# Optimization experiments

Hardware: AMD Instinct MI355X
Metric: run time of the kernel (lower is better)

The kernel has to match this reference:

```python
import jax, jax.numpy as jnp
import numpy as np

B, T, D_MODEL = 4, 2048, 2048
H, KV, HD = 16, 8, 128  # num_heads, num_kv_heads, head_dim
EPS = 1e-6


def _rope_tables(T, hd, base=10000.0):
    inv_freq = 1.0 / (base ** (np.arange(0, hd, 2, dtype=np.float32) / hd))  # [hd/2]
    ang = np.arange(T, dtype=np.float32)[:, None] * inv_freq[None, :]        # [T, hd/2]
    cos = np.repeat(np.cos(ang), 2, axis=-1)                                 # [T, hd]
    sin = np.repeat(np.sin(ang), 2, axis=-1)
    return jnp.asarray(cos), jnp.asarray(sin)


def setup_inputs() -> dict:
    key = jax.random.key(0)
    ks = jax.random.split(key, 6)
    w_std = 0.02
    x = jax.random.normal(ks[0], (B, T, D_MODEL), dtype=jnp.float32)
    Wq = jax.random.normal(ks[1], (D_MODEL, H * HD), dtype=jnp.float32) * w_std
    Wk = jax.random.normal(ks[2], (D_MODEL, KV * HD), dtype=jnp.float32) * w_std
    Wv = jax.random.normal(ks[3], (D_MODEL, KV * HD), dtype=jnp.float32) * w_std
    Wo = jax.random.normal(ks[4], (H * HD, D_MODEL), dtype=jnp.float32) * w_std
    cos, sin = _rope_tables(T, HD)
    q_gamma = jnp.ones((HD,), dtype=jnp.float32)
    k_gamma = jnp.ones((HD,), dtype=jnp.float32)
    return {"x": x, "cos": cos, "sin": sin, "Wq": Wq, "Wk": Wk, "Wv": Wv,
            "Wo": Wo, "q_gamma": q_gamma, "k_gamma": k_gamma}


def _rmsnorm(h, gamma):
    # flax nn.RMSNorm over last axis, learnable scale
    var = jnp.mean(h * h, axis=-1, keepdims=True)
    return h * jax.lax.rsqrt(var + EPS) * gamma


def _rope(h, cos, sin):
    # h: [B, T, heads, HD]; interleaved rotation
    h_rot = jnp.stack([-h[..., 1::2], h[..., 0::2]], axis=-1)
    h_rot = h_rot.reshape(h.shape)
    return h * cos[None, :, None, :] + h_rot * sin[None, :, None, :]


def reference(x, cos, sin, Wq, Wk, Wv, Wo, q_gamma, k_gamma):
    Bx, Tx, _ = x.shape
    G = H // KV  # query groups per kv head
    q = (x @ Wq).reshape(Bx, Tx, H, HD)
    k = (x @ Wk).reshape(Bx, Tx, KV, HD)
    v = (x @ Wv).reshape(Bx, Tx, KV, HD)
    q = _rope(_rmsnorm(q, q_gamma), cos, sin)
    k = _rope(_rmsnorm(k, k_gamma), cos, sin)
    scale = 1.0 / jnp.sqrt(jnp.asarray(HD, dtype=x.dtype))
    qg = q.reshape(Bx, Tx, KV, G, HD)
    # scores: [B, KV, G, Tq, Tk]
    scores = jnp.einsum('btkgd,bskd->bkgts', qg, k) * scale
    p = jax.nn.softmax(scores, axis=-1)
    o = jnp.einsum('bkgts,bskd->btkgd', p, v).reshape(Bx, Tx, H * HD)
    return o @ Wo
```

## Files before the change

### kernel.cpp

```cpp
#include <hip/hip_runtime.h>


typedef unsigned short u16;
typedef unsigned int u32;
typedef __attribute__((ext_vector_type(8))) short bf16x8;
typedef __attribute__((ext_vector_type(4))) float f32x4;

__device__ __forceinline__ float bf2f(u16 v) {
    union { u32 u; float f; } x; x.u = ((u32)v) << 16; return x.f;
}
__device__ __forceinline__ u16 f2bf(float f) {
    union { float f; u32 u; } x; x.f = f;
    u32 u = x.u;
    return (u16)((u + 0x7FFFu + ((u >> 16) & 1u)) >> 16);
}
__device__ __forceinline__ u32 packtrunc(float a, float b) {
    union { float f; u32 u; } x, y; x.f = a; y.f = b;
    return (x.u >> 16) | (y.u & 0xffff0000u);
}
__device__ __forceinline__ f32x4 mfma_bf16(bf16x8 a, bf16x8 b, f32x4 c) {
    return __builtin_amdgcn_mfma_f32_16x16x32_bf16(a, b, c, 0, 0, 0);
}
__device__ __forceinline__ void gl_lds16(const u16* g, u16* l) {
    __builtin_amdgcn_global_load_lds((const __attribute__((address_space(1))) void*)g,
                                     (__attribute__((address_space(3))) void*)l, 16, 0, 0);
}

__global__ __launch_bounds__(256)
void transpose_f2b(const float* __restrict__ in, u16* __restrict__ out, int R, int C) {
    __shared__ float tile[32][33];
    const int tx = threadIdx.x & 31, ty = threadIdx.x >> 5;
    const long c0 = (long)blockIdx.x * 32, r0 = (long)blockIdx.y * 32;
#pragma unroll
    for (int i = 0; i < 4; i++)
        tile[ty + i * 8][tx] = in[(r0 + ty + i * 8) * C + c0 + tx];
    __syncthreads();
#pragma unroll
    for (int i = 0; i < 4; i++)
        out[(c0 + ty + i * 8) * R + r0 + tx] = f2bf(tile[tx][ty + i * 8]);
}

__global__ __launch_bounds__(256)
void cast_f2b(const float* __restrict__ in, u16* __restrict__ out) {
    const long i = ((long)blockIdx.x * 256 + threadIdx.x) * 8;
    float4 a = *(const float4*)(in + i);
    float4 b = *(const float4*)(in + i + 4);
    bf16x8 v;
    v[0] = (short)f2bf(a.x); v[1] = (short)f2bf(a.y);
    v[2] = (short)f2bf(a.z); v[3] = (short)f2bf(a.w);
    v[4] = (short)f2bf(b.x); v[5] = (short)f2bf(b.y);
    v[6] = (short)f2bf(b.z); v[7] = (short)f2bf(b.w);
    *(bf16x8*)(out + i) = v;
}

__global__ __launch_bounds__(256)
void transpose_v(const u16* __restrict__ qkv, u16* __restrict__ Vt) {
    __shared__ u16 tile[32][33];
    const int tx = threadIdx.x & 31, ty = threadIdx.x >> 5;
    const int d0 = blockIdx.x * 32;
    const int tok0 = blockIdx.y * 32;
#pragma unroll
    for (int i = 0; i < 4; i++)
        tile[ty + i * 8][tx] = qkv[(long)(tok0 + ty + i * 8) * 4096 + 3072 + d0 + tx];
    __syncthreads();
    const int b = tok0 >> 11;
    const long orow = (long)b * 1024 + d0;
    const int t0 = tok0 & 2047;
#pragma unroll
    for (int i = 0; i < 4; i++)
        Vt[(orow + ty + i * 8) * 2048 + t0 + tx] = tile[tx][ty + i * 8];
}

template <bool F32OUT>
__global__ __launch_bounds__(256)
void gemm_bt_bf16(const u16* __restrict__ A, const u16* __restrict__ Bt,
                  void* __restrict__ Cp, int M, int N, int K) {
    __shared__ __align__(16) u16 As[128 * 32];
    __shared__ __align__(16) u16 Bs[128 * 32];
    const int tid = threadIdx.x, wid = tid >> 6, lane = tid & 63;
    const int q4 = lane >> 4, n16 = lane & 15;
    const int wr = (wid >> 1) * 64, wc = (wid & 1) * 64;
    const long rowT = (long)blockIdx.y * 128, colT = (long)blockIdx.x * 128;

    const int srow = wid * 32 + (lane >> 2);
    const int scol = (lane & 3) * 8;
    const u16* Ag0 = A + (rowT + srow) * K + scol;
    const u16* Ag1 = Ag0 + (long)16 * K;
    const u16* Bg0 = Bt + (colT + srow) * K + scol;
    const u16* Bg1 = Bg0 + (long)16 * K;
    u16* la0 = As + wid * 1024 + lane * 8;
    u16* la1 = la0 + 512;
    u16* lb0 = Bs + wid * 1024 + lane * 8;
    u16* lb1 = lb0 + 512;

    f32x4 acc[4][4];
#pragma unroll
    for (int i = 0; i < 4; i++)
#pragma unroll
        for (int j = 0; j < 4; j++) acc[i][j] = (f32x4){0.f, 0.f, 0.f, 0.f};

    for (int k0 = 0; k0 < K; k0 += 32) {
        gl_lds16(Ag0 + k0, la0);
        gl_lds16(Ag1 + k0, la1);
        gl_lds16(Bg0 + k0, lb0);
        gl_lds16(Bg1 + k0, lb1);
        __syncthreads();
        bf16x8 af[4], bfr[4];
#pragma unroll
        for (int mb = 0; mb < 4; mb++) af[mb]  = *(const bf16x8*)&As[(wr + mb * 16 + n16) * 32 + q4 * 8];
#pragma unroll
        for (int nb = 0; nb < 4; nb++) bfr[nb] = *(const bf16x8*)&Bs[(wc + nb * 16 + n16) * 32 + q4 * 8];
#pragma unroll
        for (int mb = 0; mb < 4; mb++)
#pragma unroll
            for (int nb = 0; nb < 4; nb++)
                acc[mb][nb] = mfma_bf16(af[mb], bfr[nb], acc[mb][nb]);
        __syncthreads();
    }

#pragma unroll
    for (int mb = 0; mb < 4; mb++)
#pragma unroll
        for (int nb = 0; nb < 4; nb++)
#pragma unroll
            for (int r = 0; r < 4; r++) {
                long row = rowT + wr + mb * 16 + q4 * 4 + r;
                long col = colT + wc + nb * 16 + n16;
                if (F32OUT) ((float*)Cp)[row * N + col] = acc[mb][nb][r];
                else        ((u16*)Cp)[row * N + col]   = f2bf(acc[mb][nb][r]);
            }
}

__global__ __launch_bounds__(256)
void rmsnorm_rope(u16* __restrict__ qkv, const float* __restrict__ cosT,
                  const float* __restrict__ sinT, const float* __restrict__ qg,
                  const float* __restrict__ kg) {
    const int w = blockIdx.x * 4 + (threadIdx.x >> 6);
    const int lane = threadIdx.x & 63;
    const int token = w / 24;
    const int hv = w - token * 24;
    const long base = (long)token * 4096 + (hv < 16 ? hv * 128 : 2048 + (hv - 16) * 128);
    const float* g = (hv < 16) ? qg : kg;
    const int t = token & 2047;

    u32 pair = *(const u32*)(qkv + base + 2 * lane);
    float a0 = bf2f((u16)(pair & 0xffffu));
    float a1 = bf2f((u16)(pair >> 16));
    float ss = a0 * a0 + a1 * a1;
#pragma unroll
    for (int off = 32; off > 0; off >>= 1) ss += __shfl_xor(ss, off);
    float rs = rsqrtf(ss * (1.0f / 128.0f) + 1e-6f);
    float h0 = a0 * rs * g[2 * lane];
    float h1 = a1 * rs * g[2 * lane + 1];
    float2 cp = *(const float2*)(cosT + (long)t * 128 + 2 * lane);
    float2 sp = *(const float2*)(sinT + (long)t * 128 + 2 * lane);
    float o0 = h0 * cp.x - h1 * sp.x;
    float o1 = h1 * cp.y + h0 * sp.y;
    if (hv < 16) {
        const float QS = 0.08838834764831845f * 1.4426950408889634f;
        o0 *= QS; o1 *= QS;
    }
    *(u32*)(qkv + base + 2 * lane) = ((u32)f2bf(o0)) | (((u32)f2bf(o1)) << 16);
}

__global__ __launch_bounds__(256)
void flash_attn(const u16* __restrict__ qkv, const u16* __restrict__ Vt,
                u16* __restrict__ attn) {
    __shared__ __align__(16) u16 Ks[2][64 * 128];
    __shared__ __align__(16) u16 Vs[2][128 * 64];
    const int tid = threadIdx.x, wid = tid >> 6, lane = tid & 63;
    const int q4 = lane >> 4, n16 = lane & 15;
    const int b = blockIdx.y >> 4, h = blockIdx.y & 15;
    const int kvh = h >> 1;
    const long rowbase = (long)b * 2048;
    const long qbase = rowbase + (long)blockIdx.x * 128 + wid * 32;

    const u16* Kbase = qkv + rowbase * 4096 + 2048 + kvh * 128;
    const u16* Vbase = Vt + ((long)(b * 8 + kvh) * 128) * 2048;

    const int krow_off = lane >> 4;
    const int kslot = lane & 15;
    int ktr[4], kgc[4];
#pragma unroll
    for (int i = 0; i < 4; i++) {
        int rho = wid * 16 + i * 4 + krow_off;
        ktr[i] = (rho & 32) | ((rho & 12) << 1) | ((rho & 16) >> 2) | (rho & 3);
        kgc[i] = kslot ^ (rho & 7);
    }
    const int vrow_off = lane >> 3;
    const int vslot = lane & 7;
    const int vg = vslot ^ vrow_off;

    auto stage = [&](int buf, int kt) {
#pragma unroll
        for (int i = 0; i < 4; i++)
            gl_lds16(Kbase + (long)(kt + ktr[i]) * 4096 + kgc[i] * 8,
                     &Ks[buf][(wid * 16 + i * 4) * 128 + lane * 8]);
#pragma unroll
        for (int i = 0; i < 4; i++) {
            int d = wid * 32 + i * 8 + vrow_off;
            gl_lds16(Vbase + (long)d * 2048 + kt + vg * 8,
                     &Vs[buf][(wid * 32 + i * 8) * 64 + lane * 8]);
        }
    };

    bf16x8 qf[2][4];
#pragma unroll
    for (int qb = 0; qb < 2; qb++) {
        const u16* p = qkv + (qbase + qb * 16 + n16) * 4096 + h * 128;
#pragma unroll
        for (int c = 0; c < 4; c++) qf[qb][c] = *(const bf16x8*)(p + c * 32 + q4 * 8);
    }

    f32x4 o[2][8];
#pragma unroll
    for (int i = 0; i < 2; i++)
#pragma unroll
        for (int j = 0; j < 8; j++) o[i][j] = (f32x4){0.f, 0.f, 0.f, 0.f};
    float l_i[2] = {0.f, 0.f};
    const float SHIFT = 18.0f;

    const int swz = n16 & 7;

    stage(0, 0);
    asm volatile("s_waitcnt vmcnt(0)" ::: "memory");
    __builtin_amdgcn_s_barrier();

    int cur = 0;
    for (int kt = 0; kt < 2048; kt += 64) {
        if (kt + 64 < 2048) stage(cur ^ 1, kt + 64);

        const u16* KsC = Ks[cur];
        const u16* VsC = Vs[cur];

        f32x4 s[2][4];
#pragma unroll
        for (int qb = 0; qb < 2; qb++)
#pragma unroll
            for (int kb = 0; kb < 4; kb++) s[qb][kb] = (f32x4){0.f, 0.f, 0.f, 0.f};
#pragma unroll
        for (int c = 0; c < 4; c++) {
            bf16x8 kf[4];
#pragma unroll
            for (int kb = 0; kb < 4; kb++) {
                int slot = (c * 4 + q4) ^ swz;
                kf[kb] = *(const bf16x8*)&KsC[(kb * 16 + n16) * 128 + slot * 8];
            }
            __builtin_amdgcn_s_setprio(1);
#pragma unroll
            for (int qb = 0; qb < 2; qb++)
#pragma unroll
                for (int kb = 0; kb < 4; kb++)
                    s[qb][kb] = mfma_bf16(kf[kb], qf[qb][c], s[qb][kb]);
            __builtin_amdgcn_s_setprio(0);
        }

        u32 pw[2][8];
#pragma unroll
        for (int qb = 0; qb < 2; qb++) {
            float sum = 0.f;
#pragma unroll
            for (int kb = 0; kb < 4; kb++) {
                float p0 = exp2f(s[qb][kb][0] - SHIFT);
                float p1 = exp2f(s[qb][kb][1] - SHIFT);
                float p2 = exp2f(s[qb][kb][2] - SHIFT);
                float p3 = exp2f(s[qb][kb][3] - SHIFT);
                sum += (p0 + p1) + (p2 + p3);
                pw[qb][kb * 2]     = packtrunc(p0, p1);
                pw[qb][kb * 2 + 1] = packtrunc(p2, p3);
            }
            l_i[qb] += sum;
        }

#pragma unroll
        for (int kc = 0; kc < 2; kc++) {
            bf16x8 vf[8];
#pragma unroll
            for (int nbh = 0; nbh < 8; nbh++) {
                int slot = (kc * 4 + q4) ^ swz;
                vf[nbh] = *(const bf16x8*)&VsC[(nbh * 16 + n16) * 64 + slot * 8];
            }
            __builtin_amdgcn_s_setprio(1);
#pragma unroll
            for (int qb = 0; qb < 2; qb++) {
                union { u32 w[4]; bf16x8 v; } pu;
                pu.w[0] = pw[qb][kc * 4];
                pu.w[1] = pw[qb][kc * 4 + 1];
                pu.w[2] = pw[qb][kc * 4 + 2];
                pu.w[3] = pw[qb][kc * 4 + 3];
#pragma unroll
                for (int nbh = 0; nbh < 8; nbh++)
                    o[qb][nbh] = mfma_bf16(pu.v, vf[nbh], o[qb][nbh]);
            }
            __builtin_amdgcn_s_setprio(0);
        }

        asm volatile("s_waitcnt vmcnt(0)" ::: "memory");
        __builtin_amdgcn_s_barrier();
        cur ^= 1;
    }

#pragma unroll
    for (int qb = 0; qb < 2; qb++) {
        l_i[qb] += __shfl_xor(l_i[qb], 16);
        l_i[qb] += __shfl_xor(l_i[qb], 32);
    }

#pragma unroll
    for (int qb = 0; qb < 2; qb++) {
        float linv = 1.0f / l_i[qb];
        float l4[4];
#pragma unroll
        for (int r = 0; r < 4; r++)
            l4[r] = __shfl(linv, (lane & 48) | (q4 * 4 + r));
#pragma unroll
        for (int r = 0; r < 4; r++) {
            u16* op = attn + (qbase + qb * 16 + q4 * 4 + r) * 2048 + h * 128 + n16;
#pragma unroll
            for (int nbh = 0; nbh < 8; nbh++)
                op[nbh * 16] = f2bf(o[qb][nbh][r] * l4[r]);
        }
    }
}

extern "C" void kernel_launch(void* const* d_in, const int* in_sizes, int n_in,
                              void* d_out, int out_size, void* d_ws, size_t ws_size,
                              hipStream_t stream) {
    const float* x    = (const float*)d_in[0];
    const float* cosT = (const float*)d_in[1];
    const float* sinT = (const float*)d_in[2];
    const float* Wq   = (const float*)d_in[3];
    const float* Wk   = (const float*)d_in[4];
    const float* Wv   = (const float*)d_in[5];
    const float* Wo   = (const float*)d_in[6];
    const float* qg   = (const float*)d_in[7];
    const float* kg   = (const float*)d_in[8];
    float* out = (float*)d_out;

    char* ws = (char*)d_ws;
    u16* Bt_qkv = (u16*)(ws);
    u16* Vt     = (u16*)(ws);
    u16* Bt_o   = (u16*)(ws + 16777216);
    u16* xb     = (u16*)(ws + 25165824);
    u16* attn   = (u16*)(ws + 25165824);
    u16* qkv    = (u16*)(ws + 58720256);

    transpose_f2b<<<dim3(64, 64), 256, 0, stream>>>(Wq, Bt_qkv, 2048, 2048);
    transpose_f2b<<<dim3(32, 64), 256, 0, stream>>>(Wk, Bt_qkv + (size_t)2048 * 2048, 2048, 1024);
    transpose_f2b<<<dim3(32, 64), 256, 0, stream>>>(Wv, Bt_qkv + (size_t)3072 * 2048, 2048, 1024);
    transpose_f2b<<<dim3(64, 64), 256, 0, stream>>>(Wo, Bt_o, 2048, 2048);
    cast_f2b<<<dim3(8192), 256, 0, stream>>>(x, xb);

    gemm_bt_bf16<false><<<dim3(32, 64), 256, 0, stream>>>(xb, Bt_qkv, qkv, 8192, 4096, 2048);

    transpose_v<<<dim3(32, 256), 256, 0, stream>>>(qkv, Vt);
    rmsnorm_rope<<<dim3(49152), 256, 0, stream>>>(qkv, cosT, sinT, qg, kg);

    flash_attn<<<dim3(16, 64), 256, 0, stream>>>(qkv, Vt, attn);

    gemm_bt_bf16<true><<<dim3(16, 64), 256, 0, stream>>>(attn, Bt_o, out, 8192, 2048, 2048);
}
```

Measured before the change: 644.0 us.

## Replace 128x128 GEMM with double-buffered swizzled 256x256 tile GEMM

Result: faster. 574.6 us (-10.8%).

```diff
diff --git a/kernel.cpp b/kernel.cpp
--- a/kernel.cpp
+++ b/kernel.cpp
@@ -72,54 +72,83 @@
 }
 
 template <bool F32OUT>
-__global__ __launch_bounds__(256)
-void gemm_bt_bf16(const u16* __restrict__ A, const u16* __restrict__ Bt,
-                  void* __restrict__ Cp, int M, int N, int K) {
-    __shared__ __align__(16) u16 As[128 * 32];
-    __shared__ __align__(16) u16 Bs[128 * 32];
+__global__ __launch_bounds__(512, 2)
+void gemm_bt_256(const u16* __restrict__ A, const u16* __restrict__ Bt,
+                 void* __restrict__ Cp, int M, int N, int K) {
+    __shared__ __align__(16) u16 As[2][256 * 64];
+    __shared__ __align__(16) u16 Bs[2][256 * 64];
     const int tid = threadIdx.x, wid = tid >> 6, lane = tid & 63;
     const int q4 = lane >> 4, n16 = lane & 15;
-    const int wr = (wid >> 1) * 64, wc = (wid & 1) * 64;
-    const long rowT = (long)blockIdx.y * 128, colT = (long)blockIdx.x * 128;
-
-    const int srow = wid * 32 + (lane >> 2);
-    const int scol = (lane & 3) * 8;
-    const u16* Ag0 = A + (rowT + srow) * K + scol;
-    const u16* Ag1 = Ag0 + (long)16 * K;
-    const u16* Bg0 = Bt + (colT + srow) * K + scol;
-    const u16* Bg1 = Bg0 + (long)16 * K;
-    u16* la0 = As + wid * 1024 + lane * 8;
-    u16* la1 = la0 + 512;
-    u16* lb0 = Bs + wid * 1024 + lane * 8;
-    u16* lb1 = lb0 + 512;
-
-    f32x4 acc[4][4];
-#pragma unroll
-    for (int i = 0; i < 4; i++)
+    const int wr = (wid >> 2) * 128;
+    const int wc = (wid & 3) * 64;
+
+    const int nbx = N >> 8;
+    const int nwg = nbx * (M >> 8);
+    int id = (int)blockIdx.x;
+    id = (id & 7) * (nwg >> 3) + (id >> 3);
+    const long rowT = (long)(id / nbx) * 256;
+    const long colT = (long)(id % nbx) * 256;
+
+    const int srow = tid >> 3;
+    const int gchunk = (tid & 7) ^ (srow & 7);
+    const u16* Ag[4]; const u16* Bg[4];
+#pragma unroll
+    for (int i = 0; i < 4; i++) {
+        Ag[i] = A  + (rowT + i * 64 + srow) * K + gchunk * 8;
+        Bg[i] = Bt + (colT + i * 64 + srow) * K + gchunk * 8;
+    }
+    const int ldst = wid * 512 + lane * 8;
+
+    auto stage = [&](int buf, int kt) {
+#pragma unroll
+        for (int i = 0; i < 4; i++)
+            gl_lds16(Ag[i] + kt, &As[buf][i * 4096 + ldst]);
+#pragma unroll
+        for (int i = 0; i < 4; i++)
+            gl_lds16(Bg[i] + kt, &Bs[buf][i * 4096 + ldst]);
+    };
+
+    f32x4 acc[8][4];
+#pragma unroll
+    for (int i = 0; i < 8; i++)
 #pragma unroll
         for (int j = 0; j < 4; j++) acc[i][j] = (f32x4){0.f, 0.f, 0.f, 0.f};
 
-    for (int k0 = 0; k0 < K; k0 += 32) {
-        gl_lds16(Ag0 + k0, la0);
-        gl_lds16(Ag1 + k0, la1);
-        gl_lds16(Bg0 + k0, lb0);
-        gl_lds16(Bg1 + k0, lb1);
-        __syncthreads();
-        bf16x8 af[4], bfr[4];
-#pragma unroll
-        for (int mb = 0; mb < 4; mb++) af[mb]  = *(const bf16x8*)&As[(wr + mb * 16 + n16) * 32 + q4 * 8];
-#pragma unroll
-        for (int nb = 0; nb < 4; nb++) bfr[nb] = *(const bf16x8*)&Bs[(wc + nb * 16 + n16) * 32 + q4 * 8];
-#pragma unroll
-        for (int mb = 0; mb < 4; mb++)
+    const int fs = n16 & 7;
+
+    stage(0, 0);
+    asm volatile("s_waitcnt vmcnt(0)" ::: "memory");
+    __builtin_amdgcn_s_barrier();
+
+    const int NT = K >> 6;
+    for (int t = 0; t < NT; ++t) {
+        const int buf = t & 1;
+        if (t + 1 < NT) stage(buf ^ 1, (t + 1) << 6);
+
+        const u16* Ac = As[buf];
+        const u16* Bc = Bs[buf];
+#pragma unroll
+        for (int kk = 0; kk < 2; kk++) {
+            const int slot = ((kk * 4 + q4) ^ fs) * 8;
+            bf16x8 af[8], bv[4];
+#pragma unroll
+            for (int mb = 0; mb < 8; mb++)
+                af[mb] = *(const bf16x8*)&Ac[(wr + mb * 16 + n16) * 64 + slot];
 #pragma unroll
             for (int nb = 0; nb < 4; nb++)
-                acc[mb][nb] = mfma_bf16(af[mb], bfr[nb], acc[mb][nb]);
-        __syncthreads();
-    }
-
-#pragma unroll
-    for (int mb = 0; mb < 4; mb++)
+                bv[nb] = *(const bf16x8*)&Bc[(wc + nb * 16 + n16) * 64 + slot];
+#pragma unroll
+            for (int mb = 0; mb < 8; mb++)
+#pragma unroll
+                for (int nb = 0; nb < 4; nb++)
+                    acc[mb][nb] = mfma_bf16(af[mb], bv[nb], acc[mb][nb]);
+        }
+        asm volatile("s_waitcnt vmcnt(0)" ::: "memory");
+        __builtin_amdgcn_s_barrier();
+    }
+
+#pragma unroll
+    for (int mb = 0; mb < 8; mb++)
 #pragma unroll
         for (int nb = 0; nb < 4; nb++)
 #pragma unroll
@@ -351,12 +380,12 @@
     transpose_f2b<<<dim3(64, 64), 256, 0, stream>>>(Wo, Bt_o, 2048, 2048);
     cast_f2b<<<dim3(8192), 256, 0, stream>>>(x, xb);
 
-    gemm_bt_bf16<false><<<dim3(32, 64), 256, 0, stream>>>(xb, Bt_qkv, qkv, 8192, 4096, 2048);
+    gemm_bt_256<false><<<dim3(512), 512, 0, stream>>>(xb, Bt_qkv, qkv, 8192, 4096, 2048);
 
     transpose_v<<<dim3(32, 256), 256, 0, stream>>>(qkv, Vt);
     rmsnorm_rope<<<dim3(49152), 256, 0, stream>>>(qkv, cosT, sinT, qg, kg);
 
     flash_attn<<<dim3(16, 64), 256, 0, stream>>>(qkv, Vt, attn);
 
-    gemm_bt_bf16<true><<<dim3(16, 64), 256, 0, stream>>>(attn, Bt_o, out, 8192, 2048, 2048);
-}
+    gemm_bt_256<true><<<dim3(256), 512, 0, stream>>>(attn, Bt_o, out, 8192, 2048, 2048);
+}
```
